# Performance work log

Measured on AMD Instinct MI355X. Metric: run time of the kernel, lower is better.

Reference implementation:

```python
import jax, jax.numpy as jnp
import numpy as np

HF8_BIAS = 14  # exponent bias for the 1-4-3 hf8 layout; HF8_MAX = 2^(15-14)*1.875 = 3.75


def hf8_decode(bits):
    """Decode 8-bit hf8 codes (1 sign, 4 exp, 3 mantissa) to float.

    Mirrors convert.hf8_to_fp16: an elementwise dequant producing the
    fp16-valued weight tensor (computed here in fp32 for reference accuracy).
    """
    bits = bits.astype(jnp.int32)
    sign = jnp.where(((bits >> 7) & 1) == 1, -1.0, 1.0)
    exp = (bits >> 3) & 0xF
    man = (bits & 0x7).astype(jnp.float32)
    normal = jnp.exp2((exp - HF8_BIAS).astype(jnp.float32)) * (1.0 + man / 8.0)
    subnormal = jnp.exp2(jnp.float32(1 - HF8_BIAS)) * (man / 8.0)
    return sign * jnp.where(exp == 0, subnormal, normal)


def setup_inputs() -> dict:
    key = jax.random.key(0)
    k1, k2, k3 = jax.random.split(key, 3)
    B, Cin, Cout, H, W, K = 8, 320, 320, 64, 64, 3
    x = jax.random.normal(k1, (B, Cin, H, W), dtype=jnp.float32)
    w_bits = jax.random.randint(k2, (Cout, Cin, K, K), 0, 256, dtype=jnp.int32)
    b_bits = jax.random.randint(k3, (Cout,), 0, 256, dtype=jnp.int32)
    return {"x": x, "w_bits": w_bits, "b_bits": b_bits}


def reference(x, w_bits, b_bits):
    # dequant hf8 -> dense weight/bias (the fusible elementwise pass)
    w = hf8_decode(w_bits)          # [Cout, Cin, K, K]
    b = hf8_decode(b_bits)          # [Cout]
    # padding_mode == 'zeros' branch: plain conv2d, stride 1, pad 1, dilation 1, groups 1
    out = jax.lax.conv_general_dilated(
        x, w,
        window_strides=(1, 1),
        padding=((1, 1), (1, 1)),
        rhs_dilation=(1, 1),
        dimension_numbers=("NCHW", "OIHW", "NCHW"),
        feature_group_count=1,
    )
    return out + b[None, :, None, None]
```

## Files before the change

kernel.cpp:

```cpp
#include <hip/hip_runtime.h>
#include <stdint.h>

typedef short v8s __attribute__((ext_vector_type(8)));
typedef float v4f __attribute__((ext_vector_type(4)));

#define CIN   320
#define COUT  320
#define HH    64
#define WW    64
#define BN    80
#define CIB   32
#define XS_C  40
#define XCOLS 66
#define XROWS 6
#define NWCH  (9*4*BN)
#define NWL   (NWCH/64)

__device__ __forceinline__ float hf8_decode_f(int b) {
    int e = (b >> 3) & 15;
    int m = b & 7;
    float v = ldexpf((float)(e ? (8 + m) : m), e ? (e - 17) : -16);
    return ((b >> 7) & 1) ? -v : v;
}

__global__ void dequant_kernel(const int* __restrict__ w_bits,
                               const int* __restrict__ b_bits,
                               unsigned short* __restrict__ w_deq,
                               float* __restrict__ b_deq) {
    int idx = blockIdx.x * 256 + threadIdx.x;
    int e    = idx & 7;
    int t    = idx >> 3;
    int co   = t % COUT;
    int t2   = t / COUT;
    int cig  = t2 % 40;
    int khkw = t2 / 40;
    int ci   = cig * 8 + e;
    float v = hf8_decode_f(w_bits[(co * CIN + ci) * 9 + khkw] & 0xFF);
    w_deq[idx] = (unsigned short)(__float_as_uint(v) >> 16);
    if (idx < COUT) b_deq[idx] = hf8_decode_f(b_bits[idx] & 0xFF);
}

__device__ __forceinline__ unsigned int cvt_pk_bf16(float lo, float hi) {
    unsigned int r;
    asm("v_cvt_pk_bf16_f32 %0, %1, %2" : "=v"(r) : "v"(lo), "v"(hi));
    return r;
}

__global__ __launch_bounds__(256, 2) void conv_mfma_kernel(
        const float* __restrict__ x,
        const unsigned short* __restrict__ w_deq,
        const float* __restrict__ b_deq,
        float* __restrict__ out) {
    __shared__ __align__(16) unsigned short xs[XROWS * XCOLS * XS_C];
    __shared__ __align__(16) unsigned short wl[NWCH * 8];

    const int tid  = threadIdx.x;
    const int bid  = blockIdx.x;
    const int cob  = bid >> 7;
    const int mb   = bid & 127;
    const int n    = mb >> 4;
    const int h0   = (mb & 15) << 2;
    const int wave = tid >> 6;
    const int lane = tid & 63;
    const int lhi  = lane >> 4;
    const int llo  = lane & 15;
    const int ciL2 = tid & 15;
    const int seg  = tid >> 4;

    for (int i = tid; i < XROWS * 2 * XS_C; i += 256) {
        int r  = i / (2 * XS_C);
        int tt = i - r * (2 * XS_C);
        int c  = (tt >= XS_C) ? 65 : 0;
        int ci = (tt >= XS_C) ? (tt - XS_C) : tt;
        xs[(r * XCOLS + c) * XS_C + ci] = 0;
    }

    v4f acc[4][5];
    #pragma unroll
    for (int i = 0; i < 4; ++i)
        #pragma unroll
        for (int j = 0; j < 5; ++j)
            acc[i][j] = (v4f){0.f, 0.f, 0.f, 0.f};

    int woff[12];
    #pragma unroll
    for (int ii = 0; ii < 12; ++ii) {
        int i = wave + ii * 4;
        if (i < NWL) {
            int c    = i * 64 + lane;
            int co   = c % BN;
            int q    = c / BN;
            int cig  = q & 3;
            int khkw = q >> 2;
            woff[ii] = ((khkw * 40 + cig) * COUT + cob * BN + co) * 16;
        } else {
            woff[ii] = 0;
        }
    }

    const float* xbase = x + ((size_t)(n * CIN) + 2 * ciL2) * (HH * WW);

    for (int t = 0; t < 10; ++t) {
        const int ci0 = t * CIB;
        __syncthreads();

        float4 xa[XROWS], xb[XROWS];
        {
            const float* xp0 = xbase + (size_t)ci0 * (HH * WW);
            const float* xp1 = xp0 + HH * WW;
            #pragma unroll
            for (int r = 0; r < XROWS; ++r) {
                int gh = h0 - 1 + r;
                if (gh >= 0 && gh < HH) {
                    xa[r] = *(const float4*)(xp0 + gh * WW + seg * 4);
                    xb[r] = *(const float4*)(xp1 + gh * WW + seg * 4);
                } else {
                    xa[r] = make_float4(0.f, 0.f, 0.f, 0.f);
                    xb[r] = make_float4(0.f, 0.f, 0.f, 0.f);
                }
            }
        }

        {
            const char* wb = (const char*)w_deq + (size_t)(ci0 >> 3) * (COUT * 16);
            #pragma unroll
            for (int ii = 0; ii < 12; ++ii) {
                int i = wave + ii * 4;
                if (i < NWL) {
                    const unsigned int* gsrc = (const unsigned int*)(wb + woff[ii]);
                    unsigned short* ldst = &wl[i * 512];
                    __builtin_amdgcn_global_load_lds(
                        (const __attribute__((address_space(1))) unsigned int*)(uintptr_t)gsrc,
                        (__attribute__((address_space(3))) unsigned int*)(uintptr_t)ldst,
                        16, 0, 0);
                }
            }
        }

        #pragma unroll
        for (int r = 0; r < XROWS; ++r) {
            unsigned int p0 = cvt_pk_bf16(xa[r].x, xb[r].x);
            unsigned int p1 = cvt_pk_bf16(xa[r].y, xb[r].y);
            unsigned int p2 = cvt_pk_bf16(xa[r].z, xb[r].z);
            unsigned int p3 = cvt_pk_bf16(xa[r].w, xb[r].w);
            int cbase = r * XCOLS + 1 + seg * 4;
            *(unsigned int*)&xs[(cbase + 0) * XS_C + 2 * ciL2] = p0;
            *(unsigned int*)&xs[(cbase + 1) * XS_C + 2 * ciL2] = p1;
            *(unsigned int*)&xs[(cbase + 2) * XS_C + 2 * ciL2] = p2;
            *(unsigned int*)&xs[(cbase + 3) * XS_C + 2 * ciL2] = p3;
        }

        __syncthreads();

        #pragma unroll
        for (int khkw = 0; khkw < 9; ++khkw) {
            const int kh = khkw / 3, kw = khkw % 3;
            v8s bfr[5];
            #pragma unroll
            for (int nr = 0; nr < 5; ++nr)
                bfr[nr] = *(const v8s*)&wl[((khkw * 4 + lhi) * BN + nr * 16 + llo) * 8];
            #pragma unroll
            for (int mr = 0; mr < 4; ++mr) {
                v8s afr = *(const v8s*)&xs[((wave + kh) * XCOLS + mr * 16 + llo + kw) * XS_C + lhi * 8];
                #pragma unroll
                for (int nr = 0; nr < 5; ++nr)
                    acc[mr][nr] = __builtin_amdgcn_mfma_f32_16x16x32_bf16(
                        afr, bfr[nr], acc[mr][nr], 0, 0, 0);
            }
        }
    }

    const int h = h0 + wave;
    #pragma unroll
    for (int nr = 0; nr < 5; ++nr) {
        int co = cob * BN + nr * 16 + llo;
        float bias = b_deq[co];
        float* op = out + ((size_t)((n * COUT + co) * HH + h)) * WW;
        #pragma unroll
        for (int mr = 0; mr < 4; ++mr) {
            int wc = mr * 16 + lhi * 4;
            float4 o;
            o.x = acc[mr][nr][0] + bias;
            o.y = acc[mr][nr][1] + bias;
            o.z = acc[mr][nr][2] + bias;
            o.w = acc[mr][nr][3] + bias;
            *(float4*)(op + wc) = o;
        }
    }
}

extern "C" void kernel_launch(void* const* d_in, const int* in_sizes, int n_in,
                              void* d_out, int out_size, void* d_ws, size_t ws_size,
                              hipStream_t stream) {
    const float* x      = (const float*)d_in[0];
    const int*   w_bits = (const int*)d_in[1];
    const int*   b_bits = (const int*)d_in[2];
    float*       out    = (float*)d_out;

    unsigned short* w_deq = (unsigned short*)d_ws;
    float*          b_deq = (float*)((char*)d_ws + (size_t)9 * 40 * COUT * 8 * 2);

    dequant_kernel<<<3600, 256, 0, stream>>>(w_bits, b_bits, w_deq, b_deq);

    conv_mfma_kernel<<<512, 256, 0, stream>>>(x, w_deq, b_deq, out);
}
```

Before: 63.71 us.

## Pre-convert input to padded bf16 channel-last layout and double-buffer weights in conv

Adds a separate pass that converts x to bf16 in a padded, channel-interleaved layout, so the conv kernel can copy input tiles with plain 16-byte loads and skip the per-tile conversion and transpose. The new conv kernel uses 512 threads with 8 output rows per block, which doubles input reuse across kernel rows. It also double-buffers the weight tiles in LDS and prefetches the next channel tile while the current one is computed. The cost is an extra kernel launch and a full read and write of x in global memory, and the new path only runs when the workspace is at least 24 MB.

New measurement: 86.32 us. 35.5% more time.

```diff
diff --git a/kernel.cpp b/kernel.cpp
--- a/kernel.cpp
+++ b/kernel.cpp
@@ -3,6 +3,7 @@
 
 typedef short v8s __attribute__((ext_vector_type(8)));
 typedef float v4f __attribute__((ext_vector_type(4)));
+typedef unsigned int u32;
 
 #define CIN   320
 #define COUT  320
@@ -10,17 +11,27 @@
 #define WW    64
 #define BN    80
 #define CIB   32
+#define NT    10
+#define XROWB 4224
+#define WBUFE 23040
+#define NWI   45
+
 #define XS_C  40
 #define XCOLS 66
 #define XROWS 6
 #define NWCH  (9*4*BN)
-#define NWL   (NWCH/64)
 
 __device__ __forceinline__ float hf8_decode_f(int b) {
     int e = (b >> 3) & 15;
     int m = b & 7;
     float v = ldexpf((float)(e ? (8 + m) : m), e ? (e - 17) : -16);
     return ((b >> 7) & 1) ? -v : v;
+}
+
+__device__ __forceinline__ u32 cvt_pk_bf16(float lo, float hi) {
+    u32 r;
+    asm("v_cvt_pk_bf16_f32 %0, %1, %2" : "=v"(r) : "v"(lo), "v"(hi));
+    return r;
 }
 
 __global__ void dequant_kernel(const int* __restrict__ w_bits,
@@ -40,10 +51,170 @@
     if (idx < COUT) b_deq[idx] = hf8_decode_f(b_bits[idx] & 0xFF);
 }
 
-__device__ __forceinline__ unsigned int cvt_pk_bf16(float lo, float hi) {
-    unsigned int r;
-    asm("v_cvt_pk_bf16_f32 %0, %1, %2" : "=v"(r) : "v"(lo), "v"(hi));
-    return r;
+__global__ __launch_bounds__(256) void convert_x_kernel(const float* __restrict__ x,
+                                                        unsigned short* __restrict__ x_t) {
+    __shared__ __align__(16) unsigned short lt[32 * 64];
+    const int b   = blockIdx.x;
+    const int hp  = b % 66;
+    const int nc  = b / 66;
+    const int tid = threadIdx.x;
+    char* outp = (char*)x_t + (size_t)b * 4096;
+    if (hp == 0 || hp == 65) {
+        *(int4*)(outp + tid * 16) = make_int4(0, 0, 0, 0);
+        return;
+    }
+    const int h = hp - 1;
+    {
+        int ci = tid >> 3, wg = tid & 7;
+        const float* src = x + ((size_t)nc * 32 + ci) * (HH * WW) + h * WW + wg * 8;
+        float4 a = *(const float4*)src;
+        float4 c = *(const float4*)(src + 4);
+        u32 d0 = cvt_pk_bf16(a.x, a.y);
+        u32 d1 = cvt_pk_bf16(a.z, a.w);
+        u32 d2 = cvt_pk_bf16(c.x, c.y);
+        u32 d3 = cvt_pk_bf16(c.z, c.w);
+        *(int4*)&lt[ci * 64 + wg * 8] = make_int4(d0, d1, d2, d3);
+    }
+    __syncthreads();
+    if (tid < 128) {
+        int w2 = tid & 31, o = tid >> 5;
+        u32 A[4], B[4];
+        #pragma unroll
+        for (int j = 0; j < 4; ++j) {
+            int p = o * 4 + j;
+            u32 de = *(const u32*)&lt[(2 * p) * 64 + w2 * 2];
+            u32 dq = *(const u32*)&lt[(2 * p + 1) * 64 + w2 * 2];
+            A[j] = __builtin_amdgcn_perm(dq, de, 0x05040100u);
+            B[j] = __builtin_amdgcn_perm(dq, de, 0x07060302u);
+        }
+        *(int4*)(outp + (2 * w2) * 64 + o * 16)     = make_int4(A[0], A[1], A[2], A[3]);
+        *(int4*)(outp + (2 * w2 + 1) * 64 + o * 16) = make_int4(B[0], B[1], B[2], B[3]);
+    }
+}
+
+__global__ __launch_bounds__(512, 2) void conv_big_kernel(
+        const unsigned short* __restrict__ x_t,
+        const unsigned short* __restrict__ w_deq,
+        const float* __restrict__ b_deq,
+        float* __restrict__ out) {
+    __shared__ __align__(16) unsigned short xs[10 * 66 * 32];
+    __shared__ __align__(16) unsigned short wl[2][WBUFE];
+
+    const int tid  = threadIdx.x;
+    const int bid  = blockIdx.x;
+    const int cob  = bid >> 6;
+    const int mb   = bid & 63;
+    const int n    = mb >> 3;
+    const int h0   = (mb & 7) << 3;
+    const int wave = tid >> 6;
+    const int lane = tid & 63;
+    const int lhi  = lane >> 4;
+    const int llo  = lane & 15;
+    const int row_base = tid >> 8;
+    const int col16    = tid & 255;
+
+    if (tid < 320) {
+        int row = tid >> 5, side = (tid >> 4) & 1, e = tid & 15;
+        *(u32*)((char*)xs + row * XROWB + side * (65 * 64) + e * 4) = 0;
+    }
+
+    int woff[6];
+    #pragma unroll
+    for (int ii = 0; ii < 6; ++ii) {
+        int i = wave + ii * 8;
+        int c = i * 64 + lane;
+        int co = c % BN;
+        int q  = c / BN;
+        int cig = q & 3, khkw = q >> 2;
+        woff[ii] = ((khkw * 40 + cig) * COUT + cob * BN + co) << 4;
+    }
+
+    v4f acc[4][5];
+    #pragma unroll
+    for (int i = 0; i < 4; ++i)
+        #pragma unroll
+        for (int j = 0; j < 5; ++j)
+            acc[i][j] = (v4f){0.f, 0.f, 0.f, 0.f};
+
+    const char* xt_base = (const char*)x_t + ((size_t)(n * NT) * 66 + h0) * 4096;
+    int4 xr[5];
+
+    auto issueW = [&](int t) {
+        unsigned short* wb = wl[t & 1];
+        const char* ws = (const char*)w_deq + (size_t)t * 4 * COUT * 16;
+        #pragma unroll
+        for (int ii = 0; ii < 6; ++ii) {
+            int i = wave + ii * 8;
+            if (i < NWI) {
+                __builtin_amdgcn_global_load_lds(
+                    (const __attribute__((address_space(1))) u32*)(uintptr_t)(ws + woff[ii]),
+                    (__attribute__((address_space(3))) u32*)(uintptr_t)((char*)wb + i * 1024),
+                    16, 0, 0);
+            }
+        }
+    };
+    auto issueX = [&](int t) {
+        const char* xb = xt_base + (size_t)t * (66 * 4096);
+        #pragma unroll
+        for (int j = 0; j < 5; ++j)
+            xr[j] = *(const int4*)(xb + (row_base + 2 * j) * 4096 + col16 * 16);
+    };
+    auto writeX = [&]() {
+        #pragma unroll
+        for (int j = 0; j < 5; ++j)
+            *(int4*)((char*)xs + (row_base + 2 * j) * XROWB + 64 + col16 * 16) = xr[j];
+    };
+    auto compute = [&](int sel) {
+        const unsigned short* wb = wl[sel];
+        #pragma unroll
+        for (int khkw = 0; khkw < 9; ++khkw) {
+            const int kh = khkw / 3, kw = khkw % 3;
+            v8s bfr[5];
+            #pragma unroll
+            for (int nr = 0; nr < 5; ++nr)
+                bfr[nr] = *(const v8s*)&wb[((khkw * 4 + lhi) * BN + nr * 16 + llo) * 8];
+            #pragma unroll
+            for (int mr = 0; mr < 4; ++mr) {
+                v8s afr = *(const v8s*)&xs[((wave + kh) * 66 + mr * 16 + llo + kw) * 32 + lhi * 8];
+                #pragma unroll
+                for (int nr = 0; nr < 5; ++nr)
+                    acc[mr][nr] = __builtin_amdgcn_mfma_f32_16x16x32_bf16(
+                        afr, bfr[nr], acc[mr][nr], 0, 0, 0);
+            }
+        }
+    };
+
+    issueW(0);
+    issueX(0);
+    __syncthreads();
+    writeX();
+    __syncthreads();
+
+    for (int t = 0; t < NT; ++t) {
+        if (t + 1 < NT) { issueW(t + 1); issueX(t + 1); }
+        compute(t & 1);
+        __syncthreads();
+        if (t + 1 < NT) writeX();
+        __syncthreads();
+    }
+
+    const int h = h0 + wave;
+    #pragma unroll
+    for (int nr = 0; nr < 5; ++nr) {
+        int co = cob * BN + nr * 16 + llo;
+        float bias = b_deq[co];
+        float* op = out + ((size_t)(n * COUT + co) * HH + h) * WW;
+        #pragma unroll
+        for (int mr = 0; mr < 4; ++mr) {
+            int wc = mr * 16 + lhi * 4;
+            float4 o;
+            o.x = acc[mr][nr][0] + bias;
+            o.y = acc[mr][nr][1] + bias;
+            o.z = acc[mr][nr][2] + bias;
+            o.w = acc[mr][nr][3] + bias;
+            *(float4*)(op + wc) = o;
+        }
+    }
 }
 
 __global__ __launch_bounds__(256, 2) void conv_mfma_kernel(
@@ -86,7 +257,7 @@
     #pragma unroll
     for (int ii = 0; ii < 12; ++ii) {
         int i = wave + ii * 4;
-        if (i < NWL) {
+        if (i < NWCH / 64) {
             int c    = i * 64 + lane;
             int co   = c % BN;
             int q    = c / BN;
@@ -120,34 +291,30 @@
                 }
             }
         }
-
         {
             const char* wb = (const char*)w_deq + (size_t)(ci0 >> 3) * (COUT * 16);
             #pragma unroll
             for (int ii = 0; ii < 12; ++ii) {
                 int i = wave + ii * 4;
-                if (i < NWL) {
-                    const unsigned int* gsrc = (const unsigned int*)(wb + woff[ii]);
-                    unsigned short* ldst = &wl[i * 512];
+                if (i < NWCH / 64) {
                     __builtin_amdgcn_global_load_lds(
-                        (const __attribute__((address_space(1))) unsigned int*)(uintptr_t)gsrc,
-                        (__attribute__((address_space(3))) unsigned int*)(uintptr_t)ldst,
+                        (const __attribute__((address_space(1))) u32*)(uintptr_t)(wb + woff[ii]),
+                        (__attribute__((address_space(3))) u32*)(uintptr_t)((char*)wl + i * 1024),
                         16, 0, 0);
                 }
             }
         }
-
         #pragma unroll
         for (int r = 0; r < XROWS; ++r) {
-            unsigned int p0 = cvt_pk_bf16(xa[r].x, xb[r].x);
-            unsigned int p1 = cvt_pk_bf16(xa[r].y, xb[r].y);
-            unsigned int p2 = cvt_pk_bf16(xa[r].z, xb[r].z);
-            unsigned int p3 = cvt_pk_bf16(xa[r].w, xb[r].w);
+            u32 p0 = cvt_pk_bf16(xa[r].x, xb[r].x);
+            u32 p1 = cvt_pk_bf16(xa[r].y, xb[r].y);
+            u32 p2 = cvt_pk_bf16(xa[r].z, xb[r].z);
+            u32 p3 = cvt_pk_bf16(xa[r].w, xb[r].w);
             int cbase = r * XCOLS + 1 + seg * 4;
-            *(unsigned int*)&xs[(cbase + 0) * XS_C + 2 * ciL2] = p0;
-            *(unsigned int*)&xs[(cbase + 1) * XS_C + 2 * ciL2] = p1;
-            *(unsigned int*)&xs[(cbase + 2) * XS_C + 2 * ciL2] = p2;
-            *(unsigned int*)&xs[(cbase + 3) * XS_C + 2 * ciL2] = p3;
+            *(u32*)&xs[(cbase + 0) * XS_C + 2 * ciL2] = p0;
+            *(u32*)&xs[(cbase + 1) * XS_C + 2 * ciL2] = p1;
+            *(u32*)&xs[(cbase + 2) * XS_C + 2 * ciL2] = p2;
+            *(u32*)&xs[(cbase + 3) * XS_C + 2 * ciL2] = p3;
         }
 
         __syncthreads();
@@ -199,8 +366,14 @@
 
     unsigned short* w_deq = (unsigned short*)d_ws;
     float*          b_deq = (float*)((char*)d_ws + (size_t)9 * 40 * COUT * 8 * 2);
+    unsigned short* x_t   = (unsigned short*)((char*)d_ws + (2u << 20));
 
     dequant_kernel<<<3600, 256, 0, stream>>>(w_bits, b_bits, w_deq, b_deq);
 
-    conv_mfma_kernel<<<512, 256, 0, stream>>>(x, w_deq, b_deq, out);
-}
+    if (ws_size >= (24ull << 20)) {
+        convert_x_kernel<<<8 * NT * 66, 256, 0, stream>>>(x, x_t);
+        conv_big_kernel<<<256, 512, 0, stream>>>(x_t, w_deq, b_deq, out);
+    } else {
+        conv_mfma_kernel<<<512, 256, 0, stream>>>(x, w_deq, b_deq, out);
+    }
+}
```
